# Performance work log

Hardware: AMD Instinct MI355X
Metric: run time of the kernel (lower is better)

## Reference

```python
import jax, jax.numpy as jnp
import numpy as np

B, T, C = 4, 2048, 1024
NH, HS = 16, 64            # n_head, head_size
BL, SL = 32, 16            # block_length, stride_length


def setup_inputs() -> dict:
    key = jax.random.key(0)
    ks = jax.random.split(key, 7)
    def lin(k, shape, fan_in):
        return jax.random.normal(k, shape, jnp.float32) * (1.0 / np.sqrt(fan_in))
    return {
        "x": jax.random.normal(ks[0], (B, T, C), jnp.float32),
        "W_attn": lin(ks[1], (3 * C, C), C),          # c_attn weight (bias=False)
        "W_proj": lin(ks[2], (C, C), C),              # c_proj weight
        "pos_emb": jax.random.normal(ks[3], (T, HS), jnp.float32) * 0.02,
        "W_fc": lin(ks[4], (4 * HS, BL * HS), BL * HS),   # compression c_fc
        "W_cproj": lin(ks[5], (HS, 4 * HS), 4 * HS),      # compression c_proj
        "ln_w": jnp.ones((HS,), jnp.float32),             # compression LayerNorm (bias=False)
    }


def _compress(h, pos_emb, W_fc, W_cproj, ln_w):
    # h: [B, nh, T, hs] -> [B, nh, num_blocks, hs] ; sliding windows of len BL, stride SL
    Bb, nh, Tt, hs = h.shape
    nb = max(1, (Tt - BL) // SL + 1)
    idx = jnp.arange(nb)[:, None] * SL + jnp.arange(BL)[None, :]        # [nb, BL]
    blocks = h[:, :, idx, :] + pos_emb[:BL][None, None, None, :, :]     # [B,nh,nb,BL,hs]
    flat = blocks.reshape(Bb, nh, nb, BL * hs)
    z = jax.nn.gelu(jnp.einsum('bnkf,gf->bnkg', flat, W_fc), approximate=False)
    z = jnp.einsum('bnkg,hg->bnkh', z, W_cproj)
    mu = jnp.mean(z, axis=-1, keepdims=True)
    var = jnp.var(z, axis=-1, keepdims=True)
    return (z - mu) / jnp.sqrt(var + 1e-5) * ln_w


def reference(x, W_attn, W_proj, pos_emb, W_fc, W_cproj, ln_w):
    Bb, Tt, Cc = x.shape
    qkv = x @ W_attn.T                                   # [B,T,3C]
    q, k, v = jnp.split(qkv, 3, axis=-1)
    q = q.reshape(Bb, Tt, NH, HS).transpose(0, 2, 1, 3)  # [B,nh,T,hs]
    k = k.reshape(Bb, Tt, NH, HS).transpose(0, 2, 1, 3)
    v = v.reshape(Bb, Tt, NH, HS).transpose(0, 2, 1, 3)

    # Computed (and discarded) exactly as in the torch forward.
    _kc = _compress(k, pos_emb, W_fc, W_cproj, ln_w)
    _vc = _compress(v, pos_emb, W_fc, W_cproj, ln_w)

    # Flash branch: is_causal=True -> attn_mask=None -> plain causal SDPA
    scale = 1.0 / np.sqrt(HS)
    scores = jnp.einsum('bhqd,bhkd->bhqk', q, k) * scale          # [B,nh,T,T]
    causal = jnp.tril(jnp.ones((Tt, Tt), dtype=bool))
    scores = jnp.where(causal, scores, -jnp.inf)
    att = jax.nn.softmax(scores, axis=-1)
    y = jnp.einsum('bhqk,bhkd->bhqd', att, v)                     # [B,nh,T,hs]
    y = y.transpose(0, 2, 1, 3).reshape(Bb, Tt, Cc)
    return y @ W_proj.T
```

## Files before the change

kernel.cpp:

```cpp
#include <hip/hip_runtime.h>
#include <hip/hip_bf16.h>
#include <stdint.h>


typedef __bf16 bf16x8 __attribute__((ext_vector_type(8)));
typedef float f32x4 __attribute__((ext_vector_type(4)));
typedef __hip_bfloat16 bf16;

#define B_ 4
#define T_ 2048
#define C_ 1024
#define NH_ 16
#define HS_ 64
#define NEG_BIG (-30000.0f)
#define SCALE_LOG2E 0.180336880111f

__device__ __forceinline__ bool detect_fp32(const unsigned short* px) {
  const int lane = threadIdx.x & 63;
  const unsigned short u = px[2 * lane];
  const int e = (u >> 7) & 0xff;
  const bool plausible = (e >= 117) && (e <= 137);
  return __popcll(__ballot(plausible)) < 32;
}

__device__ __forceinline__ void load_lds16(const bf16* g, bf16* l) {
  __builtin_amdgcn_global_load_lds(
      (const __attribute__((address_space(1))) void*)(uintptr_t)g,
      (__attribute__((address_space(3))) void*)(uintptr_t)l, 16, 0, 0);
}

__device__ __forceinline__ uint4 ld8f(const void* base, size_t elt) {
  const float* fp = (const float*)base + elt;
  float4 f0 = *(const float4*)(fp);
  float4 f1 = *(const float4*)(fp + 4);
  union { bf16 h[8]; uint4 u; } r;
  r.h[0] = __float2bfloat16(f0.x); r.h[1] = __float2bfloat16(f0.y);
  r.h[2] = __float2bfloat16(f0.z); r.h[3] = __float2bfloat16(f0.w);
  r.h[4] = __float2bfloat16(f1.x); r.h[5] = __float2bfloat16(f1.y);
  r.h[6] = __float2bfloat16(f1.z); r.h[7] = __float2bfloat16(f1.w);
  return r.u;
}

__global__ __launch_bounds__(256) void convert3(
    const void* __restrict__ x, const void* __restrict__ wa,
    const void* __restrict__ wp, bf16* __restrict__ xb, bf16* __restrict__ wab,
    bf16* __restrict__ wpb, const unsigned short* __restrict__ probe) {
  const bool f32 = detect_fp32(probe);
  int blk = blockIdx.x;
  const void* src;
  bf16* dst;
  if (blk < 4096) {
    src = x; dst = xb;
  } else if (blk < 4096 + 1536) {
    blk -= 4096; src = wa; dst = wab;
  } else {
    blk -= 4096 + 1536; src = wp; dst = wpb;
  }
  const size_t i = ((size_t)blk * 256 + threadIdx.x) * 8;
  if (f32)
    *(uint4*)(dst + i) = ld8f(src, i);
  else
    *(uint4*)(dst + i) = *(const uint4*)((const bf16*)src + i);
}

template <int IN_MODE, int OUT_MODE>
__global__ __launch_bounds__(256, 2) void gemm_bt(
    const void* __restrict__ A, const void* __restrict__ B, void* __restrict__ C,
    bf16* __restrict__ k_ws, bf16* __restrict__ v_ws,
    const unsigned short* __restrict__ in_probe,
    const unsigned short* __restrict__ out_probe, int M, int N, int K) {
  __shared__ bf16 As[128 * 32];
  __shared__ bf16 Bs[128 * 32];

  const bool f32b = in_probe ? detect_fp32(in_probe) : false;
  const bool f32a = (IN_MODE == 0) && f32b;
  const bool f32out =
      (OUT_MODE == 0) && (out_probe ? detect_fp32(out_probe) : false);

  const int tid = threadIdx.x;
  const int lane = tid & 63;
  const int wid = tid >> 6;
  const int quad = lane >> 4;
  const int col = lane & 15;
  const int m0 = blockIdx.y * 128;
  const int n0 = blockIdx.x * 128;
  const int wm = (wid >> 1) * 64;
  const int wn = (wid & 1) * 64;
  const bool vsec = (OUT_MODE == 1) && ((n0 >> 10) == 2);

  const size_t arow = (size_t)(m0 + (tid >> 2));
  const size_t brow = (size_t)(n0 + (tid >> 2));
  const int chunk = (tid & 3) * 8;

  f32x4 acc[4][4] = {};

  for (int k0 = 0; k0 < K; k0 += 32) {
    const bf16* ap0;
    const bf16* ap1;
    if (IN_MODE == 0) {
      ap0 = (const bf16*)A + arow * K + chunk + k0;
      ap1 = (const bf16*)A + (arow + 64) * K + chunk + k0;
    } else {
      const int b = m0 >> 11;
      const int tloc = (m0 & 2047) + (tid >> 2);
      const size_t aoff = ((((size_t)b * NH_) + (k0 >> 6)) * T_ + tloc) * HS_ +
                          (k0 & 32) + chunk;
      ap0 = (const bf16*)A + aoff;
      ap1 = (const bf16*)A + aoff + (size_t)64 * HS_;
    }

    uint4 a0, a1, b0, b1;
    if (f32a) {
      a0 = ld8f(A, arow * K + chunk + k0);
      a1 = ld8f(A, (arow + 64) * K + chunk + k0);
    }
    if (f32b) {
      b0 = ld8f(B, brow * K + chunk + k0);
      b1 = ld8f(B, (brow + 64) * K + chunk + k0);
    }

    __syncthreads();
    if (f32a) {
      *(uint4*)(As + tid * 8) = a0;
      *(uint4*)(As + 2048 + tid * 8) = a1;
    } else {
      load_lds16(ap0, As + tid * 8);
      load_lds16(ap1, As + 2048 + tid * 8);
    }
    if (f32b) {
      *(uint4*)(Bs + tid * 8) = b0;
      *(uint4*)(Bs + 2048 + tid * 8) = b1;
    } else {
      load_lds16((const bf16*)B + brow * K + chunk + k0, Bs + tid * 8);
      load_lds16((const bf16*)B + (brow + 64) * K + chunk + k0,
                 Bs + 2048 + tid * 8);
    }
    __syncthreads();

    bf16x8 af[4], bfr[4];
#pragma unroll
    for (int t = 0; t < 4; ++t) {
      af[t] = *(const bf16x8*)(As + (wm + t * 16 + col) * 32 + quad * 8);
      bfr[t] = *(const bf16x8*)(Bs + (wn + t * 16 + col) * 32 + quad * 8);
    }
    if (vsec) {
#pragma unroll
      for (int tm = 0; tm < 4; ++tm)
#pragma unroll
        for (int tn = 0; tn < 4; ++tn)
          acc[tm][tn] = __builtin_amdgcn_mfma_f32_16x16x32_bf16(
              bfr[tn], af[tm], acc[tm][tn], 0, 0, 0);
    } else {
#pragma unroll
      for (int tm = 0; tm < 4; ++tm)
#pragma unroll
        for (int tn = 0; tn < 4; ++tn)
          acc[tm][tn] = __builtin_amdgcn_mfma_f32_16x16x32_bf16(
              af[tm], bfr[tn], acc[tm][tn], 0, 0, 0);
    }
  }

  if (OUT_MODE == 0) {
#pragma unroll
    for (int tm = 0; tm < 4; ++tm) {
      const int mrow = m0 + wm + tm * 16 + quad * 4;
#pragma unroll
      for (int tn = 0; tn < 4; ++tn) {
        const int ncol = n0 + wn + tn * 16 + col;
#pragma unroll
        for (int r = 0; r < 4; ++r) {
          if (f32out)
            ((float*)C)[(size_t)(mrow + r) * N + ncol] = acc[tm][tn][r];
          else
            ((bf16*)C)[(size_t)(mrow + r) * N + ncol] =
                __float2bfloat16(acc[tm][tn][r]);
        }
      }
    }
  } else if (vsec) {
    const int b = m0 >> 11;
#pragma unroll
    for (int tm = 0; tm < 4; ++tm) {
      const int tloc = (m0 & 2047) + wm + tm * 16 + col;
#pragma unroll
      for (int tn = 0; tn < 4; ++tn) {
        const int vch = (n0 & (C_ - 1)) + wn + tn * 16 + quad * 4;
#pragma unroll
        for (int r = 0; r < 4; ++r) {
          const int h = (vch + r) >> 6, d = (vch + r) & 63;
          v_ws[(((size_t)b * NH_ + h) * HS_ + d) * T_ + tloc] =
              __float2bfloat16(acc[tm][tn][r]);
        }
      }
    }
  } else {
    const int sect = n0 >> 10;
    bf16* dst = (sect == 0) ? (bf16*)C : k_ws;
#pragma unroll
    for (int tm = 0; tm < 4; ++tm) {
      const int mrow = m0 + wm + tm * 16 + quad * 4;
#pragma unroll
      for (int tn = 0; tn < 4; ++tn) {
        const int c = (n0 + wn + tn * 16 + col) & (C_ - 1);
        const int h = c >> 6, d = c & 63;
#pragma unroll
        for (int r = 0; r < 4; ++r) {
          const int t = (mrow + r) & (T_ - 1);
          const int b = (mrow + r) >> 11;
          dst[(((size_t)b * NH_ + h) * T_ + t) * HS_ + d] =
              __float2bfloat16(acc[tm][tn][r]);
        }
      }
    }
  }
}

__global__ __launch_bounds__(256, 2) void attn(
    bf16* qy, const bf16* __restrict__ kws, const bf16* __restrict__ vws) {
  __shared__ bf16 Ks[64 * 72];
  __shared__ bf16 Vs[64 * 72];
  __shared__ bf16 Ps[4][32 * 72];

  const int tid = threadIdx.x;
  const int lane = tid & 63;
  const int w = tid >> 6;
  const int quad = lane >> 4;
  const int col = lane & 15;
  const int qb = (int)gridDim.x - 1 - (int)blockIdx.x;
  const int bh = blockIdx.y;
  const size_t head_off = (size_t)bh * T_ * HS_;

  const int qrow = qb * 128 + w * 32 + col;
  const bf16* qp = qy + head_off + (size_t)qrow * HS_ + quad * 8;
  bf16x8 qf0a = *(const bf16x8*)(qp);
  bf16x8 qf1a = *(const bf16x8*)(qp + 32);
  bf16x8 qf0b = *(const bf16x8*)(qp + 16 * HS_);
  bf16x8 qf1b = *(const bf16x8*)(qp + 16 * HS_ + 32);
#pragma unroll
  for (int j = 0; j < 8; ++j) {
    qf0a[j] = (__bf16)((float)qf0a[j] * SCALE_LOG2E);
    qf1a[j] = (__bf16)((float)qf1a[j] * SCALE_LOG2E);
    qf0b[j] = (__bf16)((float)qf0b[j] * SCALE_LOG2E);
    qf1b[j] = (__bf16)((float)qf1b[j] * SCALE_LOG2E);
  }

  bf16x8 onesf;
#pragma unroll
  for (int j = 0; j < 8; ++j) onesf[j] = (__bf16)1.0f;

  f32x4 oa[4] = {}, ob[4] = {};
  f32x4 lacca = {}, laccb = {};

  bf16* pw = &Ps[w][0];
  const int ntiles = 2 * (qb + 1);

  const int srow = tid >> 3, sch = tid & 7;
  const bf16* kg = kws + head_off + (size_t)srow * HS_ + sch * 8;
  const bf16* vg = vws + ((size_t)bh * HS_ + srow) * T_ + sch * 8;
  bf16* kl0 = Ks + srow * 72 + sch * 8;
  bf16* kl1 = Ks + (srow + 32) * 72 + sch * 8;
  bf16* vl0 = Vs + srow * 72 + sch * 8;
  bf16* vl1 = Vs + (srow + 32) * 72 + sch * 8;

  uint4 kr0 = *(const uint4*)(kg);
  uint4 kr1 = *(const uint4*)(kg + (size_t)32 * HS_);
  uint4 vr0 = *(const uint4*)(vg);
  uint4 vr1 = *(const uint4*)(vg + (size_t)32 * T_);

  const int qga = qb * 128 + w * 32 + col;
  const int diag_start = 2 * qb;

  for (int kt = 0; kt < ntiles; ++kt) {
    const int k0 = kt * 64;
    __syncthreads();
    *(uint4*)kl0 = kr0;
    *(uint4*)kl1 = kr1;
    *(uint4*)vl0 = vr0;
    *(uint4*)vl1 = vr1;
    __syncthreads();
    if (kt + 1 < ntiles) {
      kg += (size_t)64 * HS_;
      vg += 64;
      kr0 = *(const uint4*)(kg);
      kr1 = *(const uint4*)(kg + (size_t)32 * HS_);
      vr0 = *(const uint4*)(vg);
      vr1 = *(const uint4*)(vg + (size_t)32 * T_);
    }

    f32x4 sa[4], sb[4];
#pragma unroll
    for (int nt = 0; nt < 4; ++nt) {
      const bf16* kp = Ks + (nt * 16 + col) * 72 + quad * 8;
      bf16x8 kf0 = *(const bf16x8*)(kp);
      bf16x8 kf1 = *(const bf16x8*)(kp + 32);
      f32x4 a = {-32.0f, -32.0f, -32.0f, -32.0f};
      a = __builtin_amdgcn_mfma_f32_16x16x32_bf16(kf0, qf0a, a, 0, 0, 0);
      a = __builtin_amdgcn_mfma_f32_16x16x32_bf16(kf1, qf1a, a, 0, 0, 0);
      sa[nt] = a;
      f32x4 b = {-32.0f, -32.0f, -32.0f, -32.0f};
      b = __builtin_amdgcn_mfma_f32_16x16x32_bf16(kf0, qf0b, b, 0, 0, 0);
      b = __builtin_amdgcn_mfma_f32_16x16x32_bf16(kf1, qf1b, b, 0, 0, 0);
      sb[nt] = b;
    }

    if (kt >= diag_start) {
#pragma unroll
      for (int nt = 0; nt < 4; ++nt) {
        const int key = k0 + nt * 16 + quad * 4;
#pragma unroll
        for (int r = 0; r < 4; ++r) {
          if (key + r > qga) sa[nt][r] = NEG_BIG;
          if (key + r > qga + 16) sb[nt][r] = NEG_BIG;
        }
      }
    }

#pragma unroll
    for (int nt = 0; nt < 4; ++nt) {
      union { ushort u[4]; uint2 v; } pa, pb;
#pragma unroll
      for (int r = 0; r < 4; ++r) {
        pa.u[r] = __bfloat16_as_ushort(__float2bfloat16(exp2f(sa[nt][r])));
        pb.u[r] = __bfloat16_as_ushort(__float2bfloat16(exp2f(sb[nt][r])));
      }
      *(uint2*)(pw + col * 72 + nt * 16 + quad * 4) = pa.v;
      *(uint2*)(pw + (col + 16) * 72 + nt * 16 + quad * 4) = pb.v;
    }

    __asm__ __volatile__("s_waitcnt lgkmcnt(0)" ::: "memory");

#pragma unroll
    for (int half = 0; half < 2; ++half) {
      bf16x8 pfa = *(const bf16x8*)(pw + col * 72 + half * 32 + quad * 8);
      bf16x8 pfb = *(const bf16x8*)(pw + (col + 16) * 72 + half * 32 + quad * 8);
      lacca = __builtin_amdgcn_mfma_f32_16x16x32_bf16(pfa, onesf, lacca, 0, 0, 0);
      laccb = __builtin_amdgcn_mfma_f32_16x16x32_bf16(pfb, onesf, laccb, 0, 0, 0);
#pragma unroll
      for (int dt = 0; dt < 4; ++dt) {
        bf16x8 vf = *(const bf16x8*)(Vs + (dt * 16 + col) * 72 + half * 32 +
                                     quad * 8);
        oa[dt] = __builtin_amdgcn_mfma_f32_16x16x32_bf16(pfa, vf, oa[dt], 0, 0, 0);
        ob[dt] = __builtin_amdgcn_mfma_f32_16x16x32_bf16(pfb, vf, ob[dt], 0, 0, 0);
      }
    }
  }

  float inva[4], invb[4];
#pragma unroll
  for (int r = 0; r < 4; ++r) {
    inva[r] = 1.0f / lacca[r];
    invb[r] = 1.0f / laccb[r];
  }
#pragma unroll
  for (int dt = 0; dt < 4; ++dt)
#pragma unroll
    for (int r = 0; r < 4; ++r) {
      const int qa = qb * 128 + w * 32 + quad * 4 + r;
      qy[head_off + (size_t)qa * HS_ + dt * 16 + col] =
          __float2bfloat16(oa[dt][r] * inva[r]);
      qy[head_off + (size_t)(qa + 16) * HS_ + dt * 16 + col] =
          __float2bfloat16(ob[dt][r] * invb[r]);
    }
}

extern "C" void kernel_launch(void* const* d_in, const int* in_sizes, int n_in,
                              void* d_out, int out_size, void* d_ws, size_t ws_size,
                              hipStream_t stream) {
  const void* x = d_in[0];
  const void* W_attn = d_in[1];
  const void* W_proj = d_in[2];
  const unsigned short* probe = (const unsigned short*)d_in[0];

  const size_t qkv_elems = (size_t)B_ * NH_ * T_ * HS_;
  const size_t xe = (size_t)B_ * T_ * C_;
  const size_t wae = (size_t)3 * C_ * C_;
  const size_t wpe = (size_t)C_ * C_;

  bf16* q_ws = (bf16*)d_ws;
  bf16* k_ws = q_ws + qkv_elems;
  bf16* v_ws = k_ws + qkv_elems;
  bf16* x_bf = v_ws + qkv_elems;
  bf16* wa_bf = x_bf + xe;
  bf16* wp_bf = wa_bf + wae;
  const size_t need = (3 * qkv_elems + xe + wae + wpe) * sizeof(bf16);

  const int M = B_ * T_;

  if (ws_size >= need) {
    convert3<<<6144, 256, 0, stream>>>(x, W_attn, W_proj, x_bf, wa_bf, wp_bf,
                                       probe);
    gemm_bt<0, 1><<<dim3(3 * C_ / 128, M / 128), 256, 0, stream>>>(
        x_bf, wa_bf, q_ws, k_ws, v_ws, nullptr, nullptr, M, 3 * C_, C_);
    attn<<<dim3(T_ / 128, B_ * NH_), 256, 0, stream>>>(q_ws, k_ws, v_ws);
    gemm_bt<1, 0><<<dim3(C_ / 128, M / 128), 256, 0, stream>>>(
        q_ws, wp_bf, d_out, nullptr, nullptr, nullptr, probe, M, C_, C_);
  } else {
    gemm_bt<0, 1><<<dim3(3 * C_ / 128, M / 128), 256, 0, stream>>>(
        x, W_attn, q_ws, k_ws, v_ws, probe, nullptr, M, 3 * C_, C_);
    attn<<<dim3(T_ / 128, B_ * NH_), 256, 0, stream>>>(q_ws, k_ws, v_ws);
    gemm_bt<1, 0><<<dim3(C_ / 128, M / 128), 256, 0, stream>>>(
        q_ws, W_proj, d_out, nullptr, nullptr, probe, probe, M, C_, C_);
  }
}
```

Before: 322.9 us.

## Use single-wave attention blocks loading K/V fragments directly from global

The attention kernel now launches one 64-thread wave per 32-query chunk instead of four waves sharing a 128-query block. K and V fragments are read straight from global memory into registers, which removes the shared-memory staging and block-wide barriers. Causal tile counts become finer-grained, so less masked work is done and there are four times as many blocks for load balance. The trade-off is that K/V reuse across waves through LDS is gone, so more global/L2 traffic and exposed load latency with no prefetch.

```diff
diff --git a/kernel.cpp b/kernel.cpp
--- a/kernel.cpp
+++ b/kernel.cpp
@@ -215,22 +215,18 @@
   }
 }
 
-__global__ __launch_bounds__(256, 2) void attn(
+__global__ __launch_bounds__(64, 3) void attn(
     bf16* qy, const bf16* __restrict__ kws, const bf16* __restrict__ vws) {
-  __shared__ bf16 Ks[64 * 72];
-  __shared__ bf16 Vs[64 * 72];
-  __shared__ bf16 Ps[4][32 * 72];
-
-  const int tid = threadIdx.x;
-  const int lane = tid & 63;
-  const int w = tid >> 6;
+  __shared__ bf16 Ps[32 * 72];
+
+  const int lane = threadIdx.x & 63;
   const int quad = lane >> 4;
   const int col = lane & 15;
-  const int qb = (int)gridDim.x - 1 - (int)blockIdx.x;
+  const int qc = (int)gridDim.x - 1 - (int)blockIdx.x;
   const int bh = blockIdx.y;
   const size_t head_off = (size_t)bh * T_ * HS_;
 
-  const int qrow = qb * 128 + w * 32 + col;
+  const int qrow = qc * 32 + col;
   const bf16* qp = qy + head_off + (size_t)qrow * HS_ + quad * 8;
   bf16x8 qf0a = *(const bf16x8*)(qp);
   bf16x8 qf1a = *(const bf16x8*)(qp + 32);
@@ -251,59 +247,37 @@
   f32x4 oa[4] = {}, ob[4] = {};
   f32x4 lacca = {}, laccb = {};
 
-  bf16* pw = &Ps[w][0];
-  const int ntiles = 2 * (qb + 1);
-
-  const int srow = tid >> 3, sch = tid & 7;
-  const bf16* kg = kws + head_off + (size_t)srow * HS_ + sch * 8;
-  const bf16* vg = vws + ((size_t)bh * HS_ + srow) * T_ + sch * 8;
-  bf16* kl0 = Ks + srow * 72 + sch * 8;
-  bf16* kl1 = Ks + (srow + 32) * 72 + sch * 8;
-  bf16* vl0 = Vs + srow * 72 + sch * 8;
-  bf16* vl1 = Vs + (srow + 32) * 72 + sch * 8;
-
-  uint4 kr0 = *(const uint4*)(kg);
-  uint4 kr1 = *(const uint4*)(kg + (size_t)32 * HS_);
-  uint4 vr0 = *(const uint4*)(vg);
-  uint4 vr1 = *(const uint4*)(vg + (size_t)32 * T_);
-
-  const int qga = qb * 128 + w * 32 + col;
-  const int diag_start = 2 * qb;
+  const int ntiles = qc / 2 + 1;
+  const int qga = qc * 32 + col;
+
+  const bf16* kbase = kws + head_off + (size_t)col * HS_ + quad * 8;
+  const bf16* vbase = vws + ((size_t)bh * HS_ + col) * T_ + quad * 8;
 
   for (int kt = 0; kt < ntiles; ++kt) {
     const int k0 = kt * 64;
-    __syncthreads();
-    *(uint4*)kl0 = kr0;
-    *(uint4*)kl1 = kr1;
-    *(uint4*)vl0 = vr0;
-    *(uint4*)vl1 = vr1;
-    __syncthreads();
-    if (kt + 1 < ntiles) {
-      kg += (size_t)64 * HS_;
-      vg += 64;
-      kr0 = *(const uint4*)(kg);
-      kr1 = *(const uint4*)(kg + (size_t)32 * HS_);
-      vr0 = *(const uint4*)(vg);
-      vr1 = *(const uint4*)(vg + (size_t)32 * T_);
-    }
+
+    bf16x8 kf[4][2];
+#pragma unroll
+    for (int nt = 0; nt < 4; ++nt)
+#pragma unroll
+      for (int h = 0; h < 2; ++h)
+        kf[nt][h] =
+            *(const bf16x8*)(kbase + (size_t)(k0 + nt * 16) * HS_ + h * 32);
 
     f32x4 sa[4], sb[4];
 #pragma unroll
     for (int nt = 0; nt < 4; ++nt) {
-      const bf16* kp = Ks + (nt * 16 + col) * 72 + quad * 8;
-      bf16x8 kf0 = *(const bf16x8*)(kp);
-      bf16x8 kf1 = *(const bf16x8*)(kp + 32);
       f32x4 a = {-32.0f, -32.0f, -32.0f, -32.0f};
-      a = __builtin_amdgcn_mfma_f32_16x16x32_bf16(kf0, qf0a, a, 0, 0, 0);
-      a = __builtin_amdgcn_mfma_f32_16x16x32_bf16(kf1, qf1a, a, 0, 0, 0);
+      a = __builtin_amdgcn_mfma_f32_16x16x32_bf16(kf[nt][0], qf0a, a, 0, 0, 0);
+      a = __builtin_amdgcn_mfma_f32_16x16x32_bf16(kf[nt][1], qf1a, a, 0, 0, 0);
       sa[nt] = a;
       f32x4 b = {-32.0f, -32.0f, -32.0f, -32.0f};
-      b = __builtin_amdgcn_mfma_f32_16x16x32_bf16(kf0, qf0b, b, 0, 0, 0);
-      b = __builtin_amdgcn_mfma_f32_16x16x32_bf16(kf1, qf1b, b, 0, 0, 0);
+      b = __builtin_amdgcn_mfma_f32_16x16x32_bf16(kf[nt][0], qf0b, b, 0, 0, 0);
+      b = __builtin_amdgcn_mfma_f32_16x16x32_bf16(kf[nt][1], qf1b, b, 0, 0, 0);
       sb[nt] = b;
     }
 
-    if (kt >= diag_start) {
+    if (kt == ntiles - 1) {
 #pragma unroll
       for (int nt = 0; nt < 4; ++nt) {
         const int key = k0 + nt * 16 + quad * 4;
@@ -323,24 +297,32 @@
         pa.u[r] = __bfloat16_as_ushort(__float2bfloat16(exp2f(sa[nt][r])));
         pb.u[r] = __bfloat16_as_ushort(__float2bfloat16(exp2f(sb[nt][r])));
       }
-      *(uint2*)(pw + col * 72 + nt * 16 + quad * 4) = pa.v;
-      *(uint2*)(pw + (col + 16) * 72 + nt * 16 + quad * 4) = pb.v;
-    }
+      *(uint2*)(Ps + col * 72 + nt * 16 + quad * 4) = pa.v;
+      *(uint2*)(Ps + (col + 16) * 72 + nt * 16 + quad * 4) = pb.v;
+    }
+
+    bf16x8 vf[4][2];
+#pragma unroll
+    for (int dt = 0; dt < 4; ++dt)
+#pragma unroll
+      for (int h = 0; h < 2; ++h)
+        vf[dt][h] =
+            *(const bf16x8*)(vbase + (size_t)dt * 16 * T_ + k0 + h * 32);
 
     __asm__ __volatile__("s_waitcnt lgkmcnt(0)" ::: "memory");
 
 #pragma unroll
     for (int half = 0; half < 2; ++half) {
-      bf16x8 pfa = *(const bf16x8*)(pw + col * 72 + half * 32 + quad * 8);
-      bf16x8 pfb = *(const bf16x8*)(pw + (col + 16) * 72 + half * 32 + quad * 8);
+      bf16x8 pfa = *(const bf16x8*)(Ps + col * 72 + half * 32 + quad * 8);
+      bf16x8 pfb = *(const bf16x8*)(Ps + (col + 16) * 72 + half * 32 + quad * 8);
       lacca = __builtin_amdgcn_mfma_f32_16x16x32_bf16(pfa, onesf, lacca, 0, 0, 0);
       laccb = __builtin_amdgcn_mfma_f32_16x16x32_bf16(pfb, onesf, laccb, 0, 0, 0);
 #pragma unroll
       for (int dt = 0; dt < 4; ++dt) {
-        bf16x8 vf = *(const bf16x8*)(Vs + (dt * 16 + col) * 72 + half * 32 +
-                                     quad * 8);
-        oa[dt] = __builtin_amdgcn_mfma_f32_16x16x32_bf16(pfa, vf, oa[dt], 0, 0, 0);
-        ob[dt] = __builtin_amdgcn_mfma_f32_16x16x32_bf16(pfb, vf, ob[dt], 0, 0, 0);
+        oa[dt] = __builtin_amdgcn_mfma_f32_16x16x32_bf16(pfa, vf[dt][half],
+                                                         oa[dt], 0, 0, 0);
+        ob[dt] = __builtin_amdgcn_mfma_f32_16x16x32_bf16(pfb, vf[dt][half],
+                                                         ob[dt], 0, 0, 0);
       }
     }
   }
@@ -355,7 +337,7 @@
   for (int dt = 0; dt < 4; ++dt)
 #pragma unroll
     for (int r = 0; r < 4; ++r) {
-      const int qa = qb * 128 + w * 32 + quad * 4 + r;
+      const int qa = qc * 32 + quad * 4 + r;
       qy[head_off + (size_t)qa * HS_ + dt * 16 + col] =
           __float2bfloat16(oa[dt][r] * inva[r]);
       qy[head_off + (size_t)(qa + 16) * HS_ + dt * 16 + col] =
@@ -391,13 +373,13 @@
                                        probe);
     gemm_bt<0, 1><<<dim3(3 * C_ / 128, M / 128), 256, 0, stream>>>(
         x_bf, wa_bf, q_ws, k_ws, v_ws, nullptr, nullptr, M, 3 * C_, C_);
-    attn<<<dim3(T_ / 128, B_ * NH_), 256, 0, stream>>>(q_ws, k_ws, v_ws);
+    attn<<<dim3(T_ / 32, B_ * NH_), 64, 0, stream>>>(q_ws, k_ws, v_ws);
     gemm_bt<1, 0><<<dim3(C_ / 128, M / 128), 256, 0, stream>>>(
         q_ws, wp_bf, d_out, nullptr, nullptr, nullptr, probe, M, C_, C_);
   } else {
     gemm_bt<0, 1><<<dim3(3 * C_ / 128, M / 128), 256, 0, stream>>>(
         x, W_attn, q_ws, k_ws, v_ws, probe, nullptr, M, 3 * C_, C_);
-    attn<<<dim3(T_ / 128, B_ * NH_), 256, 0, stream>>>(q_ws, k_ws, v_ws);
+    attn<<<dim3(T_ / 32, B_ * NH_), 64, 0, stream>>>(q_ws, k_ws, v_ws);
     gemm_bt<1, 0><<<dim3(C_ / 128, M / 128), 256, 0, stream>>>(
         q_ws, W_proj, d_out, nullptr, nullptr, probe, probe, M, C_, C_);
   }
```

Result: slower. 449.2 us (+39.1%).
